# Optimization experiments

Hardware: AMD Instinct MI355X
Metric: run time of the kernel (lower is better)

The kernel has to match this reference:

```python
import jax, jax.numpy as jnp
import numpy as np
from jax.ops import segment_sum, segment_max

N = 20000   # nodes per node type (glom, imm)
E = 320000  # edges per edge type (avg degree 16)
D = 256     # feature dim (in == out, required by GIN's (1+eps)*x + aggr)
LN_EPS = 1e-5


def _ln_relu(x, gamma, beta):
    mu = jnp.mean(x, axis=-1, keepdims=True)
    var = jnp.mean((x - mu) ** 2, axis=-1, keepdims=True)
    return jax.nn.relu((x - mu) * jax.lax.rsqrt(var + LN_EPS) * gamma + beta)


def _forward(x_glom, x_imm, ew_gg, ea_ig, W_gcn, b_gcn, Wl, bl, Wr, br, att, We,
             b_gat, eps, W_gin, b_gin, gamma, beta, ei_gg, ei_ig, ei_gi):
    # ---- GCNConv on (glom->glom): add_self_loops=True, edge_weight=ew_gg ----
    src, dst = ei_gg[0], ei_gg[1]
    xw = x_glom @ W_gcn                                   # [N, D]
    deg = segment_sum(ew_gg, dst, num_segments=N) + 1.0   # +1 for self-loop weight
    dinv = jax.lax.rsqrt(deg)                             # [N]
    coef = dinv[src] * ew_gg * dinv[dst]                  # [E] symmetric gcn_norm
    out_gcn = segment_sum(coef[:, None] * xw[src], dst, num_segments=N)
    out_gcn = out_gcn + (dinv * dinv)[:, None] * xw + b_gcn  # self-loop + bias

    # ---- GATv2Conv on (imm->glom): heads=1, edge_dim=1, no self loops ----
    s, d = ei_ig[0], ei_ig[1]
    hl = x_imm @ Wl + bl          # lin_l on source  [N, D]
    hr = x_glom @ Wr + br         # lin_r on target  [N, D]
    he = ea_ig @ We               # lin_edge         [E, D]
    z = jax.nn.leaky_relu(hl[s] + hr[d] + he, 0.2)
    logits = z @ att              # [E]
    m = segment_max(logits, d, num_segments=N)            # stable segment softmax
    ex = jnp.exp(logits - m[d])
    denom = segment_sum(ex, d, num_segments=N)
    alpha = ex / denom[d]
    out_gat = segment_sum(alpha[:, None] * hl[s], d, num_segments=N) + b_gat

    # ---- GINConv on (glom->imm): nn = Linear, train_eps ----
    s2, d2 = ei_gi[0], ei_gi[1]
    agg = segment_sum(x_glom[s2], d2, num_segments=N)     # sum aggregation
    out_gin = ((1.0 + eps[0]) * x_imm + agg) @ W_gin + b_gin

    # HeteroConv(aggr='sum') across edge types per destination node type,
    # then shared LayerNorm + ReLU
    glom = _ln_relu(out_gcn + out_gat, gamma, beta)
    imm = _ln_relu(out_gin, gamma, beta)
    return glom, imm


def setup_inputs() -> dict:
    key = jax.random.key(0)
    k = jax.random.split(key, 13)
    s = 0.06  # ~ glorot-ish scale for D=256
    return {
        'x_glom': jax.random.normal(k[0], (N, D), jnp.float32),
        'x_imm': jax.random.normal(k[1], (N, D), jnp.float32),
        'ew_gg': jax.random.uniform(k[2], (E,), jnp.float32),
        'ea_ig': jax.random.normal(k[3], (E, 1), jnp.float32),
        'W_gcn': jax.random.normal(k[4], (D, D), jnp.float32) * s,
        'b_gcn': jnp.zeros((D,), jnp.float32),
        'Wl': jax.random.normal(k[5], (D, D), jnp.float32) * s,
        'bl': jnp.zeros((D,), jnp.float32),
        'Wr': jax.random.normal(k[6], (D, D), jnp.float32) * s,
        'br': jnp.zeros((D,), jnp.float32),
        'att': jax.random.normal(k[7], (D,), jnp.float32) * s,
        'We': jax.random.normal(k[8], (1, D), jnp.float32) * s,
        'b_gat': jnp.zeros((D,), jnp.float32),
        'eps': jnp.zeros((1,), jnp.float32),
        'W_gin': jax.random.normal(k[9], (D, D), jnp.float32) * s,
        'b_gin': jnp.zeros((D,), jnp.float32),
        'gamma': jnp.ones((D,), jnp.float32),
        'beta': jnp.zeros((D,), jnp.float32),
        'ei_gg': jax.random.randint(k[10], (2, E), 0, N),
        'ei_ig': jax.random.randint(k[11], (2, E), 0, N),
        'ei_gi': jax.random.randint(k[12], (2, E), 0, N),
    }


def reference(x_glom, x_imm, ew_gg, ea_ig, W_gcn, b_gcn, Wl, bl, Wr, br, att, We,
              b_gat, eps, W_gin, b_gin, gamma, beta, ei_gg, ei_ig, ei_gi):
    return _forward(x_glom, x_imm, ew_gg, ea_ig, W_gcn, b_gcn, Wl, bl, Wr, br,
                    att, We, b_gat, eps, W_gin, b_gin, gamma, beta,
                    ei_gg, ei_ig, ei_gi)
```

## Files before the change

### kernel.cpp

```cpp
#include <hip/hip_runtime.h>


constexpr int D = 256;
constexpr int EPB_LOG = 12;
constexpr int EPB = 1 << EPB_LOG;
constexpr int MAXW = 10240;

typedef __attribute__((ext_vector_type(4))) float f32x4v;
typedef __attribute__((ext_vector_type(8))) short short8;

__device__ __forceinline__ float4 ld4(const float* p) {
    return *reinterpret_cast<const float4*>(p);
}
__device__ __forceinline__ void st4(float* p, float4 v) {
    *reinterpret_cast<float4*>(p) = v;
}
__device__ __forceinline__ unsigned short f2bf(float f) {
    unsigned u = __float_as_uint(f);
    u = u + 0x7FFFu + ((u >> 16) & 1u);
    return (unsigned short)(u >> 16);
}
__device__ __forceinline__ float bf2f(unsigned short u) {
    return __uint_as_float(((unsigned)u) << 16);
}
__device__ __forceinline__ float4 ldb4(const unsigned short* p) {
    ushort4 u = *reinterpret_cast<const ushort4*>(p);
    return make_float4(bf2f(u.x), bf2f(u.y), bf2f(u.z), bf2f(u.w));
}
__device__ __forceinline__ float wave_sum(float p) {
#pragma unroll
    for (int off = 32; off > 0; off >>= 1) p += __shfl_xor(p, off, 64);
    return p;
}
__device__ __forceinline__ float gat_partial(float4 h, float4 hrv, float ea,
                                             float4 We4, float4 att4) {
    float z, pp = 0.f;
    z = h.x + hrv.x + ea * We4.x; z *= (z > 0.f) ? 1.0f : 0.2f; pp += z * att4.x;
    z = h.y + hrv.y + ea * We4.y; z *= (z > 0.f) ? 1.0f : 0.2f; pp += z * att4.y;
    z = h.z + hrv.z + ea * We4.z; z *= (z > 0.f) ? 1.0f : 0.2f; pp += z * att4.z;
    z = h.w + hrv.w + ea * We4.w; z *= (z > 0.f) ? 1.0f : 0.2f; pp += z * att4.w;
    return pp;
}

__global__ __launch_bounds__(256)
void k_front(const float* __restrict__ x_glom, const float* __restrict__ x_imm,
             unsigned short* __restrict__ xb_glom, unsigned short* __restrict__ xb_imm,
             const float* __restrict__ W0, const float* __restrict__ W1,
             const float* __restrict__ W2, const float* __restrict__ W3,
             unsigned short* __restrict__ Wt,
             const int* __restrict__ ei_gg, const int* __restrict__ ei_ig,
             const int* __restrict__ ei_gi,
             unsigned* __restrict__ blockhist, unsigned short* __restrict__ rank16,
             int n4, int nbCast, int nbH, int E, int N)
{
    __shared__ unsigned ldsh[MAXW];
    int bx = blockIdx.x;
    if (bx < 3 * nbH) {
        int t = bx / nbH;
        int b = bx - t * nbH;
        const int* ei = (t == 0) ? ei_gg : (t == 1) ? ei_ig : ei_gi;
        const int Nw = (N + 1) >> 1;
        for (int w = threadIdx.x; w < Nw; w += 256) ldsh[w] = 0u;
        __syncthreads();
        int e0 = b << EPB_LOG;
#pragma unroll
        for (int it = 0; it < EPB / 256; ++it) {
            int e = e0 + it * 256 + threadIdx.x;
            if (e < E) {
                int d = ei[E + e];
                unsigned sh = (d & 1) * 16;
                unsigned old = atomicAdd(&ldsh[d >> 1], 1u << sh);
                rank16[(size_t)t * E + e] = (unsigned short)((old >> sh) & 0xFFFFu);
            }
        }
        __syncthreads();
        unsigned* dst = blockhist + (size_t)(t * nbH + b) * Nw;
        for (int w = threadIdx.x; w < Nw; w += 256) dst[w] = ldsh[w];
        return;
    }
    bx -= 3 * nbH;
    if (bx < 2 * nbCast) {
        bool second = (bx >= nbCast);
        int i = (second ? bx - nbCast : bx) * 256 + threadIdx.x;
        if (i < n4) {
            const float* x = second ? x_imm : x_glom;
            unsigned short* y = second ? xb_imm : xb_glom;
            float4 v = ld4(x + (size_t)i * 4);
            ushort4 o;
            o.x = f2bf(v.x); o.y = f2bf(v.y); o.z = f2bf(v.z); o.w = f2bf(v.w);
            *reinterpret_cast<ushort4*>(y + (size_t)i * 4) = o;
        }
        return;
    }
    bx -= 2 * nbCast;
    {
        int w = bx >> 8;
        int i = ((bx & 255) << 8) + threadIdx.x;
        const float* W = (w == 0) ? W0 : (w == 1) ? W1 : (w == 2) ? W2 : W3;
        int c = i >> 8, k = i & 255;
        Wt[(size_t)w * D * D + i] = f2bf(W[k * D + c]);
    }
}

__device__ __forceinline__ unsigned hist_get(const unsigned* __restrict__ bh,
                                             int Nw, int nbH, int t, int b, int d)
{
    unsigned w = bh[(size_t)(t * nbH + b) * Nw + (d >> 1)];
    return (w >> ((d & 1) * 16)) & 0xFFFFu;
}

__global__ __launch_bounds__(256)
void k_scan_tile(const unsigned* __restrict__ blockhist, int* __restrict__ rows,
                 int* __restrict__ partials, int N, int TPT, int nbH)
{
    int t = blockIdx.y, tile = blockIdx.x;
    int i = tile * 256 + threadIdx.x;
    const int Nw = (N + 1) >> 1;
    __shared__ int sh[256];
    int v = 0;
    if (i < N)
        for (int b = 0; b < nbH; ++b) v += (int)hist_get(blockhist, Nw, nbH, t, b, i);
    sh[threadIdx.x] = v;
    __syncthreads();
#pragma unroll
    for (int off = 1; off < 256; off <<= 1) {
        int add = (threadIdx.x >= off) ? sh[threadIdx.x - off] : 0;
        __syncthreads();
        sh[threadIdx.x] += add;
        __syncthreads();
    }
    if (i < N) rows[(size_t)t * (N + 1) + i] = sh[threadIdx.x] - v;
    if (threadIdx.x == 255) partials[t * TPT + tile] = sh[255];
}

__global__ __launch_bounds__(128)
void k_scan_part(int* __restrict__ partials, int TPT)
{
    int t = blockIdx.x;
    __shared__ int sh[128];
    int v = (threadIdx.x < TPT) ? partials[t * TPT + threadIdx.x] : 0;
    sh[threadIdx.x] = v;
    __syncthreads();
#pragma unroll
    for (int off = 1; off < 128; off <<= 1) {
        int add = (threadIdx.x >= off) ? sh[threadIdx.x - off] : 0;
        __syncthreads();
        sh[threadIdx.x] += add;
        __syncthreads();
    }
    if (threadIdx.x < TPT) partials[t * TPT + threadIdx.x] = sh[threadIdx.x] - v;
}

__global__ void k_scan_final(int* __restrict__ rows, const int* __restrict__ partials,
                             const unsigned* __restrict__ blockhist,
                             int* __restrict__ rel32,
                             int N, int TPT, int nbH, int E)
{
    int i = blockIdx.x * 256 + threadIdx.x;
    if (i >= 3 * N) return;
    int t = i / N, j = i - t * N;
    const int Nw = (N + 1) >> 1;
    int run = rows[(size_t)t * (N + 1) + j] + partials[t * TPT + (j >> 8)];
    rows[(size_t)t * (N + 1) + j] = run;
    if (j == 0) rows[(size_t)t * (N + 1) + N] = E;
    int acc = run;
    for (int b = 0; b < nbH; ++b) {
        rel32[(size_t)(t * nbH + b) * N + j] = acc;
        acc += (int)hist_get(blockhist, Nw, nbH, t, b, j);
    }
}

__global__ __launch_bounds__(256)
void k_mid(const unsigned short* __restrict__ xbg,
           const unsigned short* __restrict__ xbi,
           const unsigned short* __restrict__ Wt,
           const float* __restrict__ br, const float* __restrict__ bl,
           unsigned short* __restrict__ xw, unsigned short* __restrict__ hr,
           unsigned short* __restrict__ hl,
           const int* __restrict__ ei_gg, const int* __restrict__ ei_ig,
           const int* __restrict__ ei_gi, const float* __restrict__ ew_gg,
           const float* __restrict__ ea_ig,
           const int* __restrict__ rel32, const unsigned short* __restrict__ rank16,
           int2* __restrict__ pk_gcn, int2* __restrict__ pk_gat,
           int* __restrict__ src_gin,
           int nbProj, int nbE, int nbH, int E, int N, int M)
{
    int bx = blockIdx.x;
    if (bx < nbProj) {
        int brow = bx / 12;
        int yy   = bx - brow * 12;
        const int lane = threadIdx.x & 63;
        const int wave = threadIdx.x >> 6;
        const int lr = lane & 15;
        const int lk = lane >> 4;
        const int row0 = brow * 256 + wave * 64;

        const unsigned short* A;
        const unsigned short* Bt0;
        int col0;
        if (yy < 8) { A = xbg; Bt0 = Wt;             col0 = yy * 64; }
        else        { A = xbi; Bt0 = Wt + 2 * D * D; col0 = (yy - 8) * 64; }

        const unsigned short* ap[4];
#pragma unroll
        for (int rf = 0; rf < 4; ++rf) {
            int arow = row0 + rf * 16 + lr;
            int arow_c = (arow < M) ? arow : (M - 1);
            ap[rf] = A + (size_t)arow_c * D + lk * 8;
        }
        const unsigned short* bp = Bt0 + (size_t)(col0 + lr) * D + lk * 8;

        f32x4v acc[4][4] = {};
#pragma unroll
        for (int k0 = 0; k0 < 256; k0 += 32) {
            short8 af[4], bf[4];
#pragma unroll
            for (int rf = 0; rf < 4; ++rf)
                af[rf] = *reinterpret_cast<const short8*>(ap[rf] + k0);
#pragma unroll
            for (int nf = 0; nf < 4; ++nf)
                bf[nf] = *reinterpret_cast<const short8*>(bp + (size_t)nf * 16 * D + k0);
#pragma unroll
            for (int rf = 0; rf < 4; ++rf)
#pragma unroll
                for (int nf = 0; nf < 4; ++nf)
                    acc[rf][nf] = __builtin_amdgcn_mfma_f32_16x16x32_bf16(
                        af[rf], bf[nf], acc[rf][nf], 0, 0, 0);
        }

#pragma unroll
        for (int nf = 0; nf < 4; ++nf) {
            int c = col0 + nf * 16 + lr;
            unsigned short* dst;
            int cc;
            float bv;
            if (yy < 8) {
                if (c < 256) { dst = xw; cc = c;       bv = 0.f;    }
                else         { dst = hr; cc = c - 256; bv = br[cc]; }
            } else           { dst = hl; cc = c;       bv = bl[cc]; }
#pragma unroll
            for (int rf = 0; rf < 4; ++rf) {
#pragma unroll
                for (int i = 0; i < 4; ++i) {
                    int r = row0 + rf * 16 + 4 * lk + i;
                    if (r < M)
                        dst[(size_t)r * D + cc] = f2bf(acc[rf][nf][i] + bv);
                }
            }
        }
        return;
    }
    int sx = bx - nbProj;
    int t = sx / nbE;
    int blk = sx - t * nbE;
    int e = blk * 256 + threadIdx.x;
    if (e >= E) return;
    int b = e >> EPB_LOG;
    const int* rel = rel32 + (size_t)(t * nbH + b) * N;
    if (t == 0) {
        int s = ei_gg[e], d = ei_gg[E + e];
        int pos = rel[d] + (int)rank16[e];
        pk_gcn[pos] = make_int2(s, __float_as_int(ew_gg[e]));
    } else if (t == 1) {
        int s = ei_ig[e], d = ei_ig[E + e];
        int pos = rel[d] + (int)rank16[(size_t)E + e];
        pk_gat[pos] = make_int2(s, __float_as_int(ea_ig[e]));
    } else {
        int s = ei_gi[e], d = ei_gi[E + e];
        int pos = rel[d] + (int)rank16[2 * (size_t)E + e];
        src_gin[pos] = s;
    }
}

__global__ void k_deg(const int* __restrict__ rows, const int2* __restrict__ pk,
                      float* __restrict__ dinv, int N)
{
    int d = blockIdx.x * 256 + threadIdx.x;
    if (d >= N) return;
    float s = 1.0f;
    int p1 = rows[d + 1];
    for (int p = rows[d]; p < p1; ++p) s += __int_as_float(pk[p].y);
    dinv[d] = rsqrtf(s);
}

__global__ __launch_bounds__(256)
void k_gin_gemm_ln(const unsigned short* __restrict__ A,
                   const unsigned short* __restrict__ Bt,
                   const float* __restrict__ bias,
                   const float* __restrict__ gamma, const float* __restrict__ beta,
                   float* __restrict__ out, int M)
{
    __shared__ float lds_s[4][64];
    __shared__ float lds_q[4][64];
    const int lane = threadIdx.x & 63;
    const int wave = threadIdx.x >> 6;
    const int lr = lane & 15;
    const int lk = lane >> 4;
    const int row0 = blockIdx.x * 64;
    const int col0 = wave * 64;

    const unsigned short* ap[4];
#pragma unroll
    for (int rf = 0; rf < 4; ++rf) {
        int arow = row0 + rf * 16 + lr;
        int arow_c = (arow < M) ? arow : (M - 1);
        ap[rf] = A + (size_t)arow_c * D + lk * 8;
    }
    const unsigned short* bp = Bt + (size_t)(col0 + lr) * D + lk * 8;

    f32x4v acc[4][4] = {};
#pragma unroll
    for (int k0 = 0; k0 < 256; k0 += 32) {
        short8 af[4], bf[4];
#pragma unroll
        for (int rf = 0; rf < 4; ++rf)
            af[rf] = *reinterpret_cast<const short8*>(ap[rf] + k0);
#pragma unroll
        for (int nf = 0; nf < 4; ++nf)
            bf[nf] = *reinterpret_cast<const short8*>(bp + (size_t)nf * 16 * D + k0);
#pragma unroll
        for (int rf = 0; rf < 4; ++rf)
#pragma unroll
            for (int nf = 0; nf < 4; ++nf)
                acc[rf][nf] = __builtin_amdgcn_mfma_f32_16x16x32_bf16(
                    af[rf], bf[nf], acc[rf][nf], 0, 0, 0);
    }

    float bv[4], gv[4], be[4];
#pragma unroll
    for (int nf = 0; nf < 4; ++nf) {
        int c = col0 + nf * 16 + lr;
        bv[nf] = bias[c]; gv[nf] = gamma[c]; be[nf] = beta[c];
    }

#pragma unroll
    for (int rf = 0; rf < 4; ++rf) {
        float ps[4], pq[4];
#pragma unroll
        for (int i = 0; i < 4; ++i) {
            float s = 0.f, q = 0.f;
#pragma unroll
            for (int nf = 0; nf < 4; ++nf) {
                float v = acc[rf][nf][i] + bv[nf];
                acc[rf][nf][i] = v;
                s += v; q += v * v;
            }
            ps[i] = s; pq[i] = q;
        }
#pragma unroll
        for (int off = 1; off < 16; off <<= 1) {
#pragma unroll
            for (int i = 0; i < 4; ++i) {
                ps[i] += __shfl_xor(ps[i], off, 64);
                pq[i] += __shfl_xor(pq[i], off, 64);
            }
        }
        if (lr == 0) {
#pragma unroll
            for (int i = 0; i < 4; ++i) {
                lds_s[wave][rf * 16 + lk * 4 + i] = ps[i];
                lds_q[wave][rf * 16 + lk * 4 + i] = pq[i];
            }
        }
    }
    __syncthreads();

#pragma unroll
    for (int rf = 0; rf < 4; ++rf) {
#pragma unroll
        for (int i = 0; i < 4; ++i) {
            int rl = rf * 16 + 4 * lk + i;
            float s = lds_s[0][rl] + lds_s[1][rl] + lds_s[2][rl] + lds_s[3][rl];
            float q = lds_q[0][rl] + lds_q[1][rl] + lds_q[2][rl] + lds_q[3][rl];
            float mu  = s * (1.0f / 256.0f);
            float var = q * (1.0f / 256.0f) - mu * mu;
            float rs  = rsqrtf(var + 1e-5f);
            int r = row0 + rl;
            if (r < M) {
#pragma unroll
                for (int nf = 0; nf < 4; ++nf) {
                    out[(size_t)r * D + col0 + nf * 16 + lr] =
                        fmaxf(0.f, (acc[rf][nf][i] - mu) * rs * gv[nf] + be[nf]);
                }
            }
        }
    }
}

__global__ __launch_bounds__(256)
void k_gather_fused(const unsigned short* __restrict__ xw,
                    const unsigned short* __restrict__ hl,
                    const unsigned short* __restrict__ hr,
                    const float* __restrict__ dinv,
                    const int* __restrict__ rows_gcn, const int2* __restrict__ pk_gcn,
                    const int* __restrict__ rows_gat, const int2* __restrict__ pk_gat,
                    const float* __restrict__ We, const float* __restrict__ att,
                    const float* __restrict__ b_gcn, const float* __restrict__ b_gat,
                    const float* __restrict__ gamma, const float* __restrict__ beta,
                    float* __restrict__ glom_out,
                    const unsigned short* __restrict__ xb_glom,
                    const float* __restrict__ x_imm, const float* __restrict__ eps,
                    const int* __restrict__ rows_gin, const int* __restrict__ src_gin,
                    unsigned short* __restrict__ agg,
                    int N)
{
    int gw   = __builtin_amdgcn_readfirstlane((blockIdx.x * 256 + threadIdx.x) >> 6);
    int lane = threadIdx.x & 63;

    if (gw < N) {
        int node = gw;
        float4 We4  = ld4(&We[lane * 4]);
        float4 att4 = ld4(&att[lane * 4]);
        float4 hrv  = ldb4(&hr[(size_t)node * D + lane * 4]);

        float di = dinv[node];
        float4 acc = ldb4(&xw[(size_t)node * D + lane * 4]);
        float4 g0  = ld4(&b_gcn[lane * 4]);
        float4 a0  = ld4(&b_gat[lane * 4]);
        float sc0 = di * di;
        acc.x = sc0 * acc.x + g0.x + a0.x;
        acc.y = sc0 * acc.y + g0.y + a0.y;
        acc.z = sc0 * acc.z + g0.z + a0.z;
        acc.w = sc0 * acc.w + g0.w + a0.w;

        int p  = rows_gcn[node];
        int p1 = rows_gcn[node + 1];
        for (; p + 4 <= p1; p += 4) {
            int2  pk[4];
            float cf[4];
            float4 v[4];
#pragma unroll
            for (int j = 0; j < 4; ++j) pk[j] = pk_gcn[p + j];
#pragma unroll
            for (int j = 0; j < 4; ++j)
                cf[j] = __int_as_float(pk[j].y) * dinv[pk[j].x] * di;
#pragma unroll
            for (int j = 0; j < 4; ++j) v[j] = ldb4(&xw[(size_t)pk[j].x * D + lane * 4]);
#pragma unroll
            for (int j = 0; j < 4; ++j) {
                acc.x += cf[j] * v[j].x; acc.y += cf[j] * v[j].y;
                acc.z += cf[j] * v[j].z; acc.w += cf[j] * v[j].w;
            }
        }
        for (; p < p1; ++p) {
            int2 pk = pk_gcn[p];
            float cx = __int_as_float(pk.y) * dinv[pk.x] * di;
            float4 v = ldb4(&xw[(size_t)pk.x * D + lane * 4]);
            acc.x += cx * v.x; acc.y += cx * v.y;
            acc.z += cx * v.z; acc.w += cx * v.w;
        }

        int q  = rows_gat[node];
        int q1 = rows_gat[node + 1];
        int has = (q1 > q);
        float den = 0.f;
        float4 ag = make_float4(0.f, 0.f, 0.f, 0.f);
        for (; q + 4 <= q1; q += 4) {
            int2  pk[4];
            float4 h[4];
            float pp[4];
#pragma unroll
            for (int j = 0; j < 4; ++j) pk[j] = pk_gat[q + j];
#pragma unroll
            for (int j = 0; j < 4; ++j) h[j] = ldb4(&hl[(size_t)pk[j].x * D + lane * 4]);
#pragma unroll
            for (int j = 0; j < 4; ++j)
                pp[j] = wave_sum(gat_partial(h[j], hrv, __int_as_float(pk[j].y), We4, att4));
            float x[4];
#pragma unroll
            for (int j = 0; j < 4; ++j) x[j] = __expf(pp[j]);
            den += (x[0] + x[1]) + (x[2] + x[3]);
#pragma unroll
            for (int j = 0; j < 4; ++j) {
                ag.x += x[j] * h[j].x; ag.y += x[j] * h[j].y;
                ag.z += x[j] * h[j].z; ag.w += x[j] * h[j].w;
            }
        }
        for (; q < q1; ++q) {
            int2 pk = pk_gat[q];
            float4 h = ldb4(&hl[(size_t)pk.x * D + lane * 4]);
            float pp = wave_sum(gat_partial(h, hrv, __int_as_float(pk.y), We4, att4));
            float x = __expf(pp);
            den += x;
            ag.x += x * h.x; ag.y += x * h.y;
            ag.z += x * h.z; ag.w += x * h.w;
        }
        if (has) {
            float inv = 1.0f / den;
            acc.x += ag.x * inv; acc.y += ag.y * inv;
            acc.z += ag.z * inv; acc.w += ag.w * inv;
        }

        float s_ = acc.x + acc.y + acc.z + acc.w;
        float sq = acc.x * acc.x + acc.y * acc.y + acc.z * acc.z + acc.w * acc.w;
#pragma unroll
        for (int off = 32; off > 0; off >>= 1) {
            s_ += __shfl_xor(s_, off, 64);
            sq += __shfl_xor(sq, off, 64);
        }
        float mu  = s_ * (1.0f / 256.0f);
        float var = sq * (1.0f / 256.0f) - mu * mu;
        float rs  = rsqrtf(var + 1e-5f);
        float4 g = ld4(&gamma[lane * 4]);
        float4 b = ld4(&beta[lane * 4]);
        float4 o;
        o.x = fmaxf(0.f, (acc.x - mu) * rs * g.x + b.x);
        o.y = fmaxf(0.f, (acc.y - mu) * rs * g.y + b.y);
        o.z = fmaxf(0.f, (acc.z - mu) * rs * g.z + b.z);
        o.w = fmaxf(0.f, (acc.w - mu) * rs * g.w + b.w);
        st4(&glom_out[(size_t)node * D + lane * 4], o);
    } else if (gw < 2 * N) {
        int node = gw - N;
        float c = 1.0f + eps[0];
        float4 acc = ld4(&x_imm[(size_t)node * D + lane * 4]);
        acc.x *= c; acc.y *= c; acc.z *= c; acc.w *= c;
        int p  = rows_gin[node];
        int p1 = rows_gin[node + 1];
        for (; p + 4 <= p1; p += 4) {
            int s[4];
            float4 v[4];
#pragma unroll
            for (int j = 0; j < 4; ++j) s[j] = src_gin[p + j];
#pragma unroll
            for (int j = 0; j < 4; ++j) v[j] = ldb4(&xb_glom[(size_t)s[j] * D + lane * 4]);
            acc.x += (v[0].x + v[1].x) + (v[2].x + v[3].x);
            acc.y += (v[0].y + v[1].y) + (v[2].y + v[3].y);
            acc.z += (v[0].z + v[1].z) + (v[2].z + v[3].z);
            acc.w += (v[0].w + v[1].w) + (v[2].w + v[3].w);
        }
        for (; p < p1; ++p) {
            int sx = src_gin[p];
            float4 v = ldb4(&xb_glom[(size_t)sx * D + lane * 4]);
            acc.x += v.x; acc.y += v.y; acc.z += v.z; acc.w += v.w;
        }
        ushort4 o;
        o.x = f2bf(acc.x); o.y = f2bf(acc.y); o.z = f2bf(acc.z); o.w = f2bf(acc.w);
        *reinterpret_cast<ushort4*>(agg + (size_t)node * D + lane * 4) = o;
    }
}

extern "C" void kernel_launch(void* const* d_in, const int* in_sizes, int n_in,
                              void* d_out, int out_size, void* d_ws, size_t ws_size,
                              hipStream_t stream)
{
    const float* x_glom = (const float*)d_in[0];
    const float* x_imm  = (const float*)d_in[1];
    const float* ew_gg  = (const float*)d_in[2];
    const float* ea_ig  = (const float*)d_in[3];
    const float* W_gcn  = (const float*)d_in[4];
    const float* b_gcn  = (const float*)d_in[5];
    const float* Wl     = (const float*)d_in[6];
    const float* bl     = (const float*)d_in[7];
    const float* Wr     = (const float*)d_in[8];
    const float* br     = (const float*)d_in[9];
    const float* att    = (const float*)d_in[10];
    const float* We     = (const float*)d_in[11];
    const float* b_gat  = (const float*)d_in[12];
    const float* eps    = (const float*)d_in[13];
    const float* W_gin  = (const float*)d_in[14];
    const float* b_gin  = (const float*)d_in[15];
    const float* gamma  = (const float*)d_in[16];
    const float* beta   = (const float*)d_in[17];
    const int*   ei_gg  = (const int*)d_in[18];
    const int*   ei_ig  = (const int*)d_in[19];
    const int*   ei_gi  = (const int*)d_in[20];

    const int N = in_sizes[0] / D;
    const int E = in_sizes[2];
    const size_t ND = (size_t)N * D;
    const int TPT = (N + 255) / 256;
    const int nbH = (E + EPB - 1) / EPB;

    char* base = (char*)d_ws;
    size_t off = 0;
    auto alloc = [&](size_t bytes) {
        void* p = base + off;
        off = (off + bytes + 255) & ~(size_t)255;
        return p;
    };
    unsigned short* xb_glom = (unsigned short*)alloc(ND * 2);
    unsigned short* xb_imm  = (unsigned short*)alloc(ND * 2);
    unsigned short* xw_b    = (unsigned short*)alloc(ND * 2);
    unsigned short* hl_b    = (unsigned short*)alloc(ND * 2);
    unsigned short* hr_b    = (unsigned short*)alloc(ND * 2);
    unsigned short* agg_b   = (unsigned short*)alloc(ND * 2);
    unsigned*       blockhist = (unsigned*)agg_b;
    unsigned short* Wt      = (unsigned short*)alloc(4 * D * D * 2);
    float* dinv    = (float*)alloc((size_t)N * 4);
    int*   rows    = (int*)alloc(3 * (size_t)(N + 1) * 4);
    int*   parts   = (int*)alloc(3 * (size_t)TPT * 4);
    int*   rel32   = (int*)alloc(3 * (size_t)nbH * N * 4);
    unsigned short* rank16 = (unsigned short*)alloc(3 * (size_t)E * 2);
    int2*  pk_gcn  = (int2*)alloc((size_t)E * 8);
    int2*  pk_gat  = (int2*)alloc((size_t)E * 8);
    int*   src_gin = (int*)alloc((size_t)E * 4);

    float* glom_out = (float*)d_out;
    float* imm_out  = (float*)d_out + ND;

    const int n4      = (int)(ND / 4);
    const int nbCast  = (n4 + 255) / 256;
    const int nbE     = (E + 255) / 256;
    const int nb_3n   = (3 * N + 255) / 256;
    const int nb_2nw  = (2 * N + 3) / 4;
    const int nbProj  = ((N + 255) / 256) * 12;

    k_front<<<3 * nbH + 2 * nbCast + 1024, 256, 0, stream>>>(
        x_glom, x_imm, xb_glom, xb_imm,
        W_gcn, Wr, Wl, W_gin, Wt,
        ei_gg, ei_ig, ei_gi,
        blockhist, rank16, n4, nbCast, nbH, E, N);
    k_scan_tile<<<dim3(TPT, 3), 256, 0, stream>>>(blockhist, rows, parts, N, TPT, nbH);
    k_scan_part<<<3, 128, 0, stream>>>(parts, TPT);
    k_scan_final<<<nb_3n, 256, 0, stream>>>(rows, parts, blockhist, rel32,
                                            N, TPT, nbH, E);
    k_mid<<<nbProj + 3 * nbE, 256, 0, stream>>>(
        xb_glom, xb_imm, Wt, br, bl, xw_b, hr_b, hl_b,
        ei_gg, ei_ig, ei_gi, ew_gg, ea_ig,
        rel32, rank16, pk_gcn, pk_gat, src_gin,
        nbProj, nbE, nbH, E, N, N);
    k_deg<<<(N + 255) / 256, 256, 0, stream>>>(rows, pk_gcn, dinv, N);
    k_gather_fused<<<nb_2nw, 256, 0, stream>>>(
        xw_b, hl_b, hr_b, dinv,
        rows, pk_gcn,
        rows + (N + 1), pk_gat,
        We, att, b_gcn, b_gat, gamma, beta, glom_out,
        xb_glom, x_imm, eps,
        rows + 2 * (N + 1), src_gin, agg_b, N);
    k_gin_gemm_ln<<<(N + 63) / 64, 256, 0, stream>>>(
        agg_b, Wt + 3 * D * D, b_gin, gamma, beta, imm_out, N);
}
```

Baseline: 226.6 us.

## Co-schedule projection GEMM with scan tiles, nontemporal scatter stores, bf16 x_imm read

Moves the projection GEMM blocks out of the scatter kernel and into the same launch as the tile-scan blocks, so the GEMM runs alongside the short scan phase rather than with the edge scatter. The scatter kernel now writes packed 64-bit edge records with nontemporal stores to keep random scattered writes from polluting cache. The GIN self term now reads the bf16 copy of x_imm instead of fp32, halving that read at some precision cost. The scan blocks must wait on the heavier GEMM blocks in one launch, which can delay the dependent scan kernels.

```diff
diff --git a/kernel.cpp b/kernel.cpp
--- a/kernel.cpp
+++ b/kernel.cpp
@@ -110,27 +110,100 @@
 }
 
 __global__ __launch_bounds__(256)
-void k_scan_tile(const unsigned* __restrict__ blockhist, int* __restrict__ rows,
-                 int* __restrict__ partials, int N, int TPT, int nbH)
-{
-    int t = blockIdx.y, tile = blockIdx.x;
-    int i = tile * 256 + threadIdx.x;
-    const int Nw = (N + 1) >> 1;
-    __shared__ int sh[256];
-    int v = 0;
-    if (i < N)
-        for (int b = 0; b < nbH; ++b) v += (int)hist_get(blockhist, Nw, nbH, t, b, i);
-    sh[threadIdx.x] = v;
-    __syncthreads();
-#pragma unroll
-    for (int off = 1; off < 256; off <<= 1) {
-        int add = (threadIdx.x >= off) ? sh[threadIdx.x - off] : 0;
+void k_scanproj(const unsigned* __restrict__ blockhist, int* __restrict__ rows,
+                int* __restrict__ partials, int N, int TPT, int nbH,
+                const unsigned short* __restrict__ xbg,
+                const unsigned short* __restrict__ xbi,
+                const unsigned short* __restrict__ Wt,
+                const float* __restrict__ br, const float* __restrict__ bl,
+                unsigned short* __restrict__ xw, unsigned short* __restrict__ hr,
+                unsigned short* __restrict__ hl, int M)
+{
+    int bx = blockIdx.x;
+    if (bx < 3 * TPT) {
+        int t = bx / TPT, tile = bx - t * TPT;
+        int i = tile * 256 + threadIdx.x;
+        const int Nw = (N + 1) >> 1;
+        __shared__ int sh[256];
+        int v = 0;
+        if (i < N)
+            for (int b = 0; b < nbH; ++b)
+                v += (int)hist_get(blockhist, Nw, nbH, t, b, i);
+        sh[threadIdx.x] = v;
         __syncthreads();
-        sh[threadIdx.x] += add;
-        __syncthreads();
-    }
-    if (i < N) rows[(size_t)t * (N + 1) + i] = sh[threadIdx.x] - v;
-    if (threadIdx.x == 255) partials[t * TPT + tile] = sh[255];
+#pragma unroll
+        for (int off = 1; off < 256; off <<= 1) {
+            int add = (threadIdx.x >= off) ? sh[threadIdx.x - off] : 0;
+            __syncthreads();
+            sh[threadIdx.x] += add;
+            __syncthreads();
+        }
+        if (i < N) rows[(size_t)t * (N + 1) + i] = sh[threadIdx.x] - v;
+        if (threadIdx.x == 255) partials[t * TPT + tile] = sh[255];
+        return;
+    }
+    int pp = bx - 3 * TPT;
+    int brow = pp / 12;
+    int yy   = pp - brow * 12;
+    const int lane = threadIdx.x & 63;
+    const int wave = threadIdx.x >> 6;
+    const int lr = lane & 15;
+    const int lk = lane >> 4;
+    const int row0 = brow * 256 + wave * 64;
+
+    const unsigned short* A;
+    const unsigned short* Bt0;
+    int col0;
+    if (yy < 8) { A = xbg; Bt0 = Wt;             col0 = yy * 64; }
+    else        { A = xbi; Bt0 = Wt + 2 * D * D; col0 = (yy - 8) * 64; }
+
+    const unsigned short* ap[4];
+#pragma unroll
+    for (int rf = 0; rf < 4; ++rf) {
+        int arow = row0 + rf * 16 + lr;
+        int arow_c = (arow < M) ? arow : (M - 1);
+        ap[rf] = A + (size_t)arow_c * D + lk * 8;
+    }
+    const unsigned short* bp = Bt0 + (size_t)(col0 + lr) * D + lk * 8;
+
+    f32x4v acc[4][4] = {};
+#pragma unroll
+    for (int k0 = 0; k0 < 256; k0 += 32) {
+        short8 af[4], bf[4];
+#pragma unroll
+        for (int rf = 0; rf < 4; ++rf)
+            af[rf] = *reinterpret_cast<const short8*>(ap[rf] + k0);
+#pragma unroll
+        for (int nf = 0; nf < 4; ++nf)
+            bf[nf] = *reinterpret_cast<const short8*>(bp + (size_t)nf * 16 * D + k0);
+#pragma unroll
+        for (int rf = 0; rf < 4; ++rf)
+#pragma unroll
+            for (int nf = 0; nf < 4; ++nf)
+                acc[rf][nf] = __builtin_amdgcn_mfma_f32_16x16x32_bf16(
+                    af[rf], bf[nf], acc[rf][nf], 0, 0, 0);
+    }
+
+#pragma unroll
+    for (int nf = 0; nf < 4; ++nf) {
+        int c = col0 + nf * 16 + lr;
+        unsigned short* dst;
+        int cc;
+        float bv;
+        if (yy < 8) {
+            if (c < 256) { dst = xw; cc = c;       bv = 0.f;    }
+            else         { dst = hr; cc = c - 256; bv = br[cc]; }
+        } else           { dst = hl; cc = c;       bv = bl[cc]; }
+#pragma unroll
+        for (int rf = 0; rf < 4; ++rf) {
+#pragma unroll
+            for (int i = 0; i < 4; ++i) {
+                int r = row0 + rf * 16 + 4 * lk + i;
+                if (r < M)
+                    dst[(size_t)r * D + cc] = f2bf(acc[rf][nf][i] + bv);
+            }
+        }
+    }
 }
 
 __global__ __launch_bounds__(128)
@@ -171,88 +244,16 @@
 }
 
 __global__ __launch_bounds__(256)
-void k_mid(const unsigned short* __restrict__ xbg,
-           const unsigned short* __restrict__ xbi,
-           const unsigned short* __restrict__ Wt,
-           const float* __restrict__ br, const float* __restrict__ bl,
-           unsigned short* __restrict__ xw, unsigned short* __restrict__ hr,
-           unsigned short* __restrict__ hl,
-           const int* __restrict__ ei_gg, const int* __restrict__ ei_ig,
-           const int* __restrict__ ei_gi, const float* __restrict__ ew_gg,
-           const float* __restrict__ ea_ig,
-           const int* __restrict__ rel32, const unsigned short* __restrict__ rank16,
-           int2* __restrict__ pk_gcn, int2* __restrict__ pk_gat,
-           int* __restrict__ src_gin,
-           int nbProj, int nbE, int nbH, int E, int N, int M)
+void k_scatter(const int* __restrict__ ei_gg, const int* __restrict__ ei_ig,
+               const int* __restrict__ ei_gi, const float* __restrict__ ew_gg,
+               const float* __restrict__ ea_ig,
+               const int* __restrict__ rel32, const unsigned short* __restrict__ rank16,
+               long long* __restrict__ pk_gcn, long long* __restrict__ pk_gat,
+               int* __restrict__ src_gin, int nbE, int nbH, int E, int N)
 {
     int bx = blockIdx.x;
-    if (bx < nbProj) {
-        int brow = bx / 12;
-        int yy   = bx - brow * 12;
-        const int lane = threadIdx.x & 63;
-        const int wave = threadIdx.x >> 6;
-        const int lr = lane & 15;
-        const int lk = lane >> 4;
-        const int row0 = brow * 256 + wave * 64;
-
-        const unsigned short* A;
-        const unsigned short* Bt0;
-        int col0;
-        if (yy < 8) { A = xbg; Bt0 = Wt;             col0 = yy * 64; }
-        else        { A = xbi; Bt0 = Wt + 2 * D * D; col0 = (yy - 8) * 64; }
-
-        const unsigned short* ap[4];
-#pragma unroll
-        for (int rf = 0; rf < 4; ++rf) {
-            int arow = row0 + rf * 16 + lr;
-            int arow_c = (arow < M) ? arow : (M - 1);
-            ap[rf] = A + (size_t)arow_c * D + lk * 8;
-        }
-        const unsigned short* bp = Bt0 + (size_t)(col0 + lr) * D + lk * 8;
-
-        f32x4v acc[4][4] = {};
-#pragma unroll
-        for (int k0 = 0; k0 < 256; k0 += 32) {
-            short8 af[4], bf[4];
-#pragma unroll
-            for (int rf = 0; rf < 4; ++rf)
-                af[rf] = *reinterpret_cast<const short8*>(ap[rf] + k0);
-#pragma unroll
-            for (int nf = 0; nf < 4; ++nf)
-                bf[nf] = *reinterpret_cast<const short8*>(bp + (size_t)nf * 16 * D + k0);
-#pragma unroll
-            for (int rf = 0; rf < 4; ++rf)
-#pragma unroll
-                for (int nf = 0; nf < 4; ++nf)
-                    acc[rf][nf] = __builtin_amdgcn_mfma_f32_16x16x32_bf16(
-                        af[rf], bf[nf], acc[rf][nf], 0, 0, 0);
-        }
-
-#pragma unroll
-        for (int nf = 0; nf < 4; ++nf) {
-            int c = col0 + nf * 16 + lr;
-            unsigned short* dst;
-            int cc;
-            float bv;
-            if (yy < 8) {
-                if (c < 256) { dst = xw; cc = c;       bv = 0.f;    }
-                else         { dst = hr; cc = c - 256; bv = br[cc]; }
-            } else           { dst = hl; cc = c;       bv = bl[cc]; }
-#pragma unroll
-            for (int rf = 0; rf < 4; ++rf) {
-#pragma unroll
-                for (int i = 0; i < 4; ++i) {
-                    int r = row0 + rf * 16 + 4 * lk + i;
-                    if (r < M)
-                        dst[(size_t)r * D + cc] = f2bf(acc[rf][nf][i] + bv);
-                }
-            }
-        }
-        return;
-    }
-    int sx = bx - nbProj;
-    int t = sx / nbE;
-    int blk = sx - t * nbE;
+    int t = bx / nbE;
+    int blk = bx - t * nbE;
     int e = blk * 256 + threadIdx.x;
     if (e >= E) return;
     int b = e >> EPB_LOG;
@@ -260,15 +261,19 @@
     if (t == 0) {
         int s = ei_gg[e], d = ei_gg[E + e];
         int pos = rel[d] + (int)rank16[e];
-        pk_gcn[pos] = make_int2(s, __float_as_int(ew_gg[e]));
+        long long v = ((long long)(unsigned)__float_as_uint(ew_gg[e]) << 32)
+                    | (unsigned)s;
+        __builtin_nontemporal_store(v, &pk_gcn[pos]);
     } else if (t == 1) {
         int s = ei_ig[e], d = ei_ig[E + e];
         int pos = rel[d] + (int)rank16[(size_t)E + e];
-        pk_gat[pos] = make_int2(s, __float_as_int(ea_ig[e]));
+        long long v = ((long long)(unsigned)__float_as_uint(ea_ig[e]) << 32)
+                    | (unsigned)s;
+        __builtin_nontemporal_store(v, &pk_gat[pos]);
     } else {
         int s = ei_gi[e], d = ei_gi[E + e];
         int pos = rel[d] + (int)rank16[2 * (size_t)E + e];
-        src_gin[pos] = s;
+        __builtin_nontemporal_store(s, &src_gin[pos]);
     }
 }
 
@@ -399,7 +404,8 @@
                     const float* __restrict__ gamma, const float* __restrict__ beta,
                     float* __restrict__ glom_out,
                     const unsigned short* __restrict__ xb_glom,
-                    const float* __restrict__ x_imm, const float* __restrict__ eps,
+                    const unsigned short* __restrict__ xb_imm,
+                    const float* __restrict__ eps,
                     const int* __restrict__ rows_gin, const int* __restrict__ src_gin,
                     unsigned short* __restrict__ agg,
                     int N)
@@ -512,7 +518,7 @@
     } else if (gw < 2 * N) {
         int node = gw - N;
         float c = 1.0f + eps[0];
-        float4 acc = ld4(&x_imm[(size_t)node * D + lane * 4]);
+        float4 acc = ldb4(&xb_imm[(size_t)node * D + lane * 4]);
         acc.x *= c; acc.y *= c; acc.z *= c; acc.w *= c;
         int p  = rows_gin[node];
         int p1 = rows_gin[node + 1];
@@ -610,22 +616,23 @@
         W_gcn, Wr, Wl, W_gin, Wt,
         ei_gg, ei_ig, ei_gi,
         blockhist, rank16, n4, nbCast, nbH, E, N);
-    k_scan_tile<<<dim3(TPT, 3), 256, 0, stream>>>(blockhist, rows, parts, N, TPT, nbH);
+    k_scanproj<<<3 * TPT + nbProj, 256, 0, stream>>>(
+        blockhist, rows, parts, N, TPT, nbH,
+        xb_glom, xb_imm, Wt, br, bl, xw_b, hr_b, hl_b, N);
     k_scan_part<<<3, 128, 0, stream>>>(parts, TPT);
     k_scan_final<<<nb_3n, 256, 0, stream>>>(rows, parts, blockhist, rel32,
                                             N, TPT, nbH, E);
-    k_mid<<<nbProj + 3 * nbE, 256, 0, stream>>>(
-        xb_glom, xb_imm, Wt, br, bl, xw_b, hr_b, hl_b,
+    k_scatter<<<3 * nbE, 256, 0, stream>>>(
         ei_gg, ei_ig, ei_gi, ew_gg, ea_ig,
-        rel32, rank16, pk_gcn, pk_gat, src_gin,
-        nbProj, nbE, nbH, E, N, N);
+        rel32, rank16, (long long*)pk_gcn, (long long*)pk_gat, src_gin,
+        nbE, nbH, E, N);
     k_deg<<<(N + 255) / 256, 256, 0, stream>>>(rows, pk_gcn, dinv, N);
     k_gather_fused<<<nb_2nw, 256, 0, stream>>>(
         xw_b, hl_b, hr_b, dinv,
         rows, pk_gcn,
         rows + (N + 1), pk_gat,
         We, att, b_gcn, b_gat, gamma, beta, glom_out,
-        xb_glom, x_imm, eps,
+        xb_glom, xb_imm, eps,
         rows + 2 * (N + 1), src_gin, agg_b, N);
     k_gin_gemm_ln<<<(N + 63) / 64, 256, 0, stream>>>(
         agg_b, Wt + 3 * D * D, b_gin, gamma, beta, imm_out, N);
```

Measured after the change: 239.9 us. 5.9% more time.
